# Optimization experiments

Hardware: AMD Instinct MI355X
Metric: run time of the kernel (lower is better)

## Reference

```python
import jax, jax.numpy as jnp
import numpy as np

BSZ, SEQ, DIM = 2, 2048, 4096
N_HEADS, N_KV_HEADS, HEAD_DIM = 32, 8, 128
N_REP = N_HEADS // N_KV_HEADS
MAX_BS, MAX_SEQ = 4, 2048
ROPE_THETA = 500000.0


def setup_inputs() -> dict:
    key = jax.random.key(0)
    ks = jax.random.split(key, 6)
    sc = 1.0 / np.sqrt(DIM)
    x = jax.random.normal(ks[0], (BSZ, SEQ, DIM), jnp.float32)
    wq = jax.random.normal(ks[1], (DIM, N_HEADS * HEAD_DIM), jnp.float32) * sc
    wk = jax.random.normal(ks[2], (DIM, N_KV_HEADS * HEAD_DIM), jnp.float32) * sc
    wv = jax.random.normal(ks[3], (DIM, N_KV_HEADS * HEAD_DIM), jnp.float32) * sc
    wo = jax.random.normal(ks[4], (N_HEADS * HEAD_DIM, DIM), jnp.float32) * sc
    cache_k = jnp.zeros((MAX_BS, MAX_SEQ, N_KV_HEADS, HEAD_DIM), jnp.float32)
    cache_v = jnp.zeros((MAX_BS, MAX_SEQ, N_KV_HEADS, HEAD_DIM), jnp.float32)
    # precomputed rotary frequencies (freqs_cis = cos + i*sin)
    inv = 1.0 / (ROPE_THETA ** (np.arange(0, HEAD_DIM, 2, dtype=np.float32) / HEAD_DIM))
    t = np.arange(SEQ, dtype=np.float32)
    freqs = np.outer(t, inv)  # [SEQ, HEAD_DIM//2]
    freqs_cos = jnp.asarray(np.cos(freqs), jnp.float32)
    freqs_sin = jnp.asarray(np.sin(freqs), jnp.float32)
    # causal additive mask, broadcast over (batch, heads)
    neg = jnp.full((SEQ, SEQ), -1e9, jnp.float32)
    mask = jnp.triu(neg, k=1)[None, None, :, :]
    return {"x": x, "wq": wq, "wk": wk, "wv": wv, "wo": wo,
            "cache_k": cache_k, "cache_v": cache_v,
            "freqs_cos": freqs_cos, "freqs_sin": freqs_sin,
            "mask": mask, "start_pos": 0}


def _apply_rope(t, cos, sin):
    # t: [b, s, h, d]; complex multiply on (even, odd) pairs
    b, s, h, d = t.shape
    tr = t.reshape(b, s, h, d // 2, 2)
    a, bb = tr[..., 0], tr[..., 1]
    cos = cos[None, :, None, :]
    sin = sin[None, :, None, :]
    out = jnp.stack([a * cos - bb * sin, a * sin + bb * cos], axis=-1)
    return out.reshape(b, s, h, d)


def reference(x, wq, wk, wv, wo, cache_k, cache_v, freqs_cos, freqs_sin, mask, start_pos):
    bsz, seqlen, _ = x.shape
    xq = (x @ wq).reshape(bsz, seqlen, N_HEADS, HEAD_DIM)
    xk = (x @ wk).reshape(bsz, seqlen, N_KV_HEADS, HEAD_DIM)
    xv = (x @ wv).reshape(bsz, seqlen, N_KV_HEADS, HEAD_DIM)
    xq = _apply_rope(xq, freqs_cos, freqs_sin)
    xk = _apply_rope(xk, freqs_cos, freqs_sin)
    # KV-cache append (start_pos is a static Python int)
    cache_k = jax.lax.dynamic_update_slice(cache_k, xk, (0, start_pos, 0, 0))
    cache_v = jax.lax.dynamic_update_slice(cache_v, xv, (0, start_pos, 0, 0))
    keys = cache_k[:bsz, : start_pos + seqlen]    # [b, kv_len, kvh, d]
    values = cache_v[:bsz, : start_pos + seqlen]
    # GQA repeat_kv: tile kv heads n_rep times -> [b, kv_len, H, d]
    keys = jnp.repeat(keys, N_REP, axis=2)
    values = jnp.repeat(values, N_REP, axis=2)
    q = xq.transpose(0, 2, 1, 3)        # [b, H, s, d]
    k = keys.transpose(0, 2, 1, 3)      # [b, H, kv, d]
    v = values.transpose(0, 2, 1, 3)
    scores = jnp.einsum('bhqd,bhkd->bhqk', q, k) / np.sqrt(HEAD_DIM)
    if mask is not None:
        scores = scores + mask
    probs = jax.nn.softmax(scores.astype(jnp.float32), axis=-1).astype(q.dtype)
    out = jnp.einsum('bhqk,bhkd->bhqd', probs, v)
    out = out.transpose(0, 2, 1, 3).reshape(bsz, seqlen, -1)
    return out @ wo
```

## Files before the change

kernel.cpp:

```cpp
#include <hip/hip_runtime.h>
#include <hip/hip_bf16.h>
#include <cstdint>

typedef __attribute__((ext_vector_type(8))) __bf16 bf16x8;
typedef __attribute__((ext_vector_type(4))) __bf16 bf16x4;
typedef __attribute__((ext_vector_type(2))) __bf16 bf16x2;
typedef __attribute__((ext_vector_type(4))) float  f32x4;

#define MFMA16(a,b,c) __builtin_amdgcn_mfma_f32_16x16x32_bf16((a),(b),(c),0,0,0)

__device__ __forceinline__ void gl16(const void* g, void* l) {
  __builtin_amdgcn_global_load_lds(
      (const __attribute__((address_space(1))) void*)g,
      (__attribute__((address_space(3))) void*)l, 16, 0, 0);
}

static constexpr int BSZ = 2, SEQ = 2048, DIM = 4096;
static constexpr int NH = 32, NKV = 8, HD = 128;
static constexpr int TOK = BSZ * SEQ;
static constexpr int NQKV = NH*HD + 2*NKV*HD;
static constexpr float QSCALE = 0.08838834764831845f;
static constexpr float FNEG = -3.0e38f;

__global__ __launch_bounds__(256) void f32_to_bf16_k(const float* __restrict__ in,
                                                     __bf16* __restrict__ out) {
  int i = (blockIdx.x * 256 + threadIdx.x) * 4;
  float4 v = *(const float4*)(in + i);
  bf16x4 o = { (__bf16)v.x, (__bf16)v.y, (__bf16)v.z, (__bf16)v.w };
  *(bf16x4*)(out + i) = o;
}

__global__ __launch_bounds__(256) void wtrans64_k(const float* __restrict__ S,
                                                  __bf16* __restrict__ D, int sC) {
  __shared__ __align__(16) __bf16 t[64 * 66];
  const int tid = threadIdx.x;
  const int cb = blockIdx.x, rb = blockIdx.y;
#pragma unroll
  for (int i = 0; i < 16; ++i) {
    int e = i * 256 + tid; int r = e >> 6, c = e & 63;
    t[c * 66 + r] = (__bf16)S[(size_t)(rb * 64 + r) * sC + cb * 64 + c];
  }
  __syncthreads();
#pragma unroll
  for (int i = 0; i < 16; ++i) {
    int e = i * 256 + tid; int c = e >> 6, r = e & 63;
    D[(size_t)(cb * 64 + c) * 4096 + rb * 64 + r] = t[c * 66 + r];
  }
}

__global__ __launch_bounds__(256) void gemm_bf16_bt_k(const __bf16* __restrict__ A,
                                                      const __bf16* __restrict__ Bt,
                                                      float* __restrict__ C,
                                                      int M, int N, int K) {
  __shared__ __align__(16) __bf16 lA[128 * 64];
  __shared__ __align__(16) __bf16 lB[128 * 64];
  const int tid = threadIdx.x, lane = tid & 63, wid = tid >> 6;
  const int bm = blockIdx.y, bn = blockIdx.x;
  const int wm = wid & 1, wn = wid >> 1;
  f32x4 acc[4][4] = {};

  const int srow = lane >> 3, scol = lane & 7;
  const __bf16* Ag = A + ((size_t)bm * 128 + wid * 8 + srow) * K + scol * 8;
  const __bf16* Bg = Bt + ((size_t)bn * 128 + wid * 8 + srow) * K + scol * 8;
  __bf16* lAw = lA + wid * 512;
  __bf16* lBw = lB + wid * 512;

  const int nk = K >> 6;
  for (int kt = 0; kt < nk; ++kt) {
    const __bf16* ag = Ag + (size_t)kt * 64;
    const __bf16* bg = Bg + (size_t)kt * 64;
#pragma unroll
    for (int i = 0; i < 4; ++i) {
      gl16(ag + (size_t)i * 32 * K, lAw + i * 2048);
      gl16(bg + (size_t)i * 32 * K, lBw + i * 2048);
    }
    __syncthreads();
#pragma unroll
    for (int kk = 0; kk < 2; ++kk) {
      bf16x8 af[4], bfv[4];
#pragma unroll
      for (int m = 0; m < 4; ++m)
        af[m] = *(const bf16x8*)&lA[(wm * 64 + m * 16 + (lane & 15)) * 64 + kk * 32 + (lane >> 4) * 8];
#pragma unroll
      for (int n = 0; n < 4; ++n)
        bfv[n] = *(const bf16x8*)&lB[(wn * 64 + n * 16 + (lane & 15)) * 64 + kk * 32 + (lane >> 4) * 8];
#pragma unroll
      for (int m = 0; m < 4; ++m)
#pragma unroll
        for (int n = 0; n < 4; ++n)
          acc[m][n] = MFMA16(af[m], bfv[n], acc[m][n]);
    }
    __syncthreads();
  }
  const int r0 = (lane >> 4) * 4, cN = lane & 15;
#pragma unroll
  for (int m = 0; m < 4; ++m) {
    size_t row = (size_t)bm * 128 + wm * 64 + m * 16 + r0;
#pragma unroll
    for (int n = 0; n < 4; ++n) {
      size_t col = (size_t)bn * 128 + wn * 64 + n * 16 + cN;
#pragma unroll
      for (int r = 0; r < 4; ++r)
        C[(row + r) * N + col] = acc[m][n][r];
    }
  }
}

__global__ __launch_bounds__(256) void rope_qk_k(const float* __restrict__ QKV,
                                                 const float* __restrict__ fc,
                                                 const float* __restrict__ fs,
                                                 __bf16* __restrict__ Qb,
                                                 __bf16* __restrict__ Kb) {
  int idx = blockIdx.x * 256 + threadIdx.x;
  int tok = idx / 2560;
  int rem = idx - tok * 2560;
  int head = rem >> 6, p = rem & 63;
  int b = tok >> 11, s = tok & 2047;
  float2 v = *(const float2*)(QKV + (size_t)tok * NQKV + head * 128 + 2 * p);
  float c = fc[s * 64 + p], sn = fs[s * 64 + p];
  float x = v.x * c - v.y * sn;
  float y = v.x * sn + v.y * c;
  if (head < 32) {
    x *= QSCALE; y *= QSCALE;
    bf16x2 o = { (__bf16)x, (__bf16)y };
    *(bf16x2*)(Qb + ((size_t)(b * 32 + head) * 2048 + s) * 128 + 2 * p) = o;
  } else {
    bf16x2 o = { (__bf16)x, (__bf16)y };
    *(bf16x2*)(Kb + ((size_t)(b * 8 + head - 32) * 2048 + s) * 128 + 2 * p) = o;
  }
}

__global__ __launch_bounds__(256) void vtrans_k(const float* __restrict__ QKV,
                                                __bf16* __restrict__ Vt) {
  __shared__ __align__(16) __bf16 t[128 * 66];
  const int sb = blockIdx.x, hk = blockIdx.y, b = blockIdx.z;
  const int tid = threadIdx.x;
#pragma unroll
  for (int i = 0; i < 32; ++i) {
    int e = i * 256 + tid; int s = e >> 7, d = e & 127;
    t[d * 66 + s] = (__bf16)QKV[(size_t)(b * 2048 + sb * 64 + s) * NQKV + 5120 + hk * 128 + d];
  }
  __syncthreads();
  int d = tid >> 1, s0 = (tid & 1) * 32;
  __bf16* dst = Vt + ((size_t)(b * 8 + hk) * 128 + d) * 2048 + sb * 64 + s0;
  const unsigned* srcu = (const unsigned*)&t[d * 66 + s0];
  unsigned* dstu = (unsigned*)dst;
#pragma unroll
  for (int i = 0; i < 16; ++i) dstu[i] = srcu[i];
}

__global__ __launch_bounds__(256) void attn64_k(const __bf16* __restrict__ Q,
                                                const __bf16* __restrict__ Kc,
                                                const __bf16* __restrict__ Vt,
                                                __bf16* __restrict__ Ab) {
  __shared__ __align__(16) __bf16 lK[64 * 128];
  __shared__ __align__(16) __bf16 lV[128 * 64];
  __shared__ __align__(16) __bf16 lP[4][16 * 64];
  const int qt = gridDim.x - 1 - blockIdx.x;
  const int h = blockIdx.y, b = blockIdx.z;
  const int hk = h >> 2;
  const int tid = threadIdx.x, lane = tid & 63, wid = tid >> 6;
  const int qb = qt * 64;
  const int lo = lane & 15, hi = lane >> 4;
  const int xk = (lo & 7) * 8;
  const __bf16* Qp = Q + ((size_t)(b * 32 + h) * 2048 + qb) * 128;
  const __bf16* Kp = Kc + (size_t)(b * 8 + hk) * 2048 * 128;
  const __bf16* Vp = Vt + (size_t)(b * 8 + hk) * 128 * 2048;

  bf16x8 qf[4];
#pragma unroll
  for (int kq = 0; kq < 4; ++kq)
    qf[kq] = *(const bf16x8*)(Qp + (size_t)(wid * 16 + lo) * 128 + kq * 32 + hi * 8);

  f32x4 accO[8] = {};
  float mr[4] = { FNEG, FNEG, FNEG, FNEG };
  float lr[4] = { 0.f, 0.f, 0.f, 0.f };

  const int srow16 = lane >> 4, scol16 = lane & 15;
  const int srow8 = lane >> 3, scol8 = lane & 7;

  for (int kb = 0; kb <= qt; ++kb) {
#pragma unroll
    for (int i = 0; i < 4; ++i) {
      const int krow = (i * 4 + wid) * 4 + srow16;
      gl16(Kp + (size_t)(kb * 64 + krow) * 128 + (scol16 ^ (krow & 7)) * 8,
           (__bf16*)lK + (i * 4 + wid) * 512);
      const int vrow = (i * 4 + wid) * 8 + srow8;
      gl16(Vp + (size_t)vrow * 2048 + kb * 64 + (scol8 ^ srow8) * 8,
           (__bf16*)lV + (i * 4 + wid) * 512);
    }
    __syncthreads();

    f32x4 sc[4] = {};
    __builtin_amdgcn_s_setprio(1);
#pragma unroll
    for (int nb = 0; nb < 4; ++nb)
#pragma unroll
      for (int kk = 0; kk < 4; ++kk) {
        bf16x8 kf = *(const bf16x8*)&lK[(nb * 16 + lo) * 128 + ((kk * 32 + hi * 8) ^ xk)];
        sc[nb] = MFMA16(qf[kk], kf, sc[nb]);
      }
    __builtin_amdgcn_s_setprio(0);

    const bool lastb = (kb == qt);
    const int qrow0 = qb + wid * 16 + hi * 4;
    const int kcol0 = kb * 64 + lo;
    float tm[4] = { FNEG, FNEG, FNEG, FNEG };
#pragma unroll
    for (int nb = 0; nb < 4; ++nb)
#pragma unroll
      for (int r = 0; r < 4; ++r) {
        float s = sc[nb][r];
        if (lastb && (kcol0 + nb * 16 > qrow0 + r)) s = FNEG;
        sc[nb][r] = s;
        tm[r] = fmaxf(tm[r], s);
      }
#pragma unroll
    for (int r = 0; r < 4; ++r) {
#pragma unroll
      for (int off = 1; off < 16; off <<= 1)
        tm[r] = fmaxf(tm[r], __shfl_xor(tm[r], off));
      float mn = fmaxf(mr[r], tm[r]);
      tm[r] = __expf(mr[r] - mn);
      mr[r] = mn;
    }
    float rs[4] = { 0.f, 0.f, 0.f, 0.f };
#pragma unroll
    for (int nb = 0; nb < 4; ++nb)
#pragma unroll
      for (int r = 0; r < 4; ++r) {
        float p = __expf(sc[nb][r] - mr[r]);
        rs[r] += p;
        const int q = hi * 4 + r;
        lP[wid][q * 64 + ((nb * 16 + lo) ^ ((q & 7) * 8))] = (__bf16)p;
      }
#pragma unroll
    for (int r = 0; r < 4; ++r) {
#pragma unroll
      for (int off = 1; off < 16; off <<= 1)
        rs[r] += __shfl_xor(rs[r], off);
      lr[r] = lr[r] * tm[r] + rs[r];
    }
#pragma unroll
    for (int nb2 = 0; nb2 < 8; ++nb2)
#pragma unroll
      for (int r = 0; r < 4; ++r)
        accO[nb2][r] *= tm[r];

    __syncthreads();

    __builtin_amdgcn_s_setprio(1);
#pragma unroll
    for (int kk = 0; kk < 2; ++kk) {
      bf16x8 pf = *(const bf16x8*)&lP[wid][lo * 64 + ((kk * 32 + hi * 8) ^ xk)];
#pragma unroll
      for (int nb2 = 0; nb2 < 8; ++nb2) {
        bf16x8 vf = *(const bf16x8*)&lV[(nb2 * 16 + lo) * 64 + ((kk * 32 + hi * 8) ^ xk)];
        accO[nb2] = MFMA16(pf, vf, accO[nb2]);
      }
    }
    __builtin_amdgcn_s_setprio(0);
    __syncthreads();
  }

  float inv[4];
#pragma unroll
  for (int r = 0; r < 4; ++r) inv[r] = 1.0f / lr[r];
#pragma unroll
  for (int nb2 = 0; nb2 < 8; ++nb2)
#pragma unroll
    for (int r = 0; r < 4; ++r)
      Ab[((size_t)b * 2048 + qb + wid * 16 + hi * 4 + r) * 4096 + h * 128 + nb2 * 16 + lo] =
          (__bf16)(accO[nb2][r] * inv[r]);
}

extern "C" void kernel_launch(void* const* d_in, const int* in_sizes, int n_in,
                              void* d_out, int out_size, void* d_ws, size_t ws_size,
                              hipStream_t stream) {
  const float* x  = (const float*)d_in[0];
  const float* wq = (const float*)d_in[1];
  const float* wk = (const float*)d_in[2];
  const float* wv = (const float*)d_in[3];
  const float* wo = (const float*)d_in[4];
  const float* fc = (const float*)d_in[7];
  const float* fs = (const float*)d_in[8];
  float* out = (float*)d_out;

  char* ws = (char*)d_ws;
  __bf16* Wqkvt = (__bf16*)(ws + 0);
  __bf16* Wot   = (__bf16*)(ws + 50331648);
  __bf16* Qb    = (__bf16*)(ws + 83886080);
  __bf16* Kb    = (__bf16*)(ws + 117440512);
  __bf16* Vtb   = (__bf16*)(ws + 125829120);
  __bf16* Xbf   = (__bf16*)(ws + 134217728);
  float*  QKVf  = (float*)(ws + 167772160);
  __bf16* Ab    = (__bf16*)(ws + 167772160);

  f32_to_bf16_k<<<TOK * DIM / 1024, 256, 0, stream>>>(x, Xbf);
  wtrans64_k<<<dim3(64, 64), 256, 0, stream>>>(wq, Wqkvt, 4096);
  wtrans64_k<<<dim3(16, 64), 256, 0, stream>>>(wk, Wqkvt + (size_t)4096 * 4096, 1024);
  wtrans64_k<<<dim3(16, 64), 256, 0, stream>>>(wv, Wqkvt + (size_t)5120 * 4096, 1024);
  wtrans64_k<<<dim3(64, 64), 256, 0, stream>>>(wo, Wot, 4096);

  gemm_bf16_bt_k<<<dim3(48, 32), 256, 0, stream>>>(Xbf, Wqkvt, QKVf, TOK, NQKV, DIM);

  rope_qk_k<<<TOK * 40 * 64 / 256, 256, 0, stream>>>(QKVf, fc, fs, Qb, Kb);
  vtrans_k<<<dim3(32, 8, 2), 256, 0, stream>>>(QKVf, Vtb);

  attn64_k<<<dim3(32, 32, 2), 256, 0, stream>>>(Qb, Kb, Vtb, Ab);

  gemm_bf16_bt_k<<<dim3(32, 32), 256, 0, stream>>>(Ab, Wot, out, TOK, DIM, DIM);
}
```

Measured before the change: 1.175 ms.

## Process 128-query tiles per block with double-buffered K/V prefetch

The attention kernel now handles two 64-row query sub-tiles per block, so each K/V tile loaded into LDS is reused twice. It double-buffers the K and V tiles, issuing the next tile's global-to-LDS load before computing on the current one, and drops one barrier per iteration. The cost is more registers (two accumulator sets) and more LDS. Causal work per block is also less balanced, and the grid has half as many blocks.

```diff
diff --git a/kernel.cpp b/kernel.cpp
--- a/kernel.cpp
+++ b/kernel.cpp
@@ -149,129 +149,150 @@
   for (int i = 0; i < 16; ++i) dstu[i] = srcu[i];
 }
 
-__global__ __launch_bounds__(256) void attn64_k(const __bf16* __restrict__ Q,
-                                                const __bf16* __restrict__ Kc,
-                                                const __bf16* __restrict__ Vt,
-                                                __bf16* __restrict__ Ab) {
-  __shared__ __align__(16) __bf16 lK[64 * 128];
-  __shared__ __align__(16) __bf16 lV[128 * 64];
+__global__ __launch_bounds__(256, 2) void attn128_k(const __bf16* __restrict__ Q,
+                                                    const __bf16* __restrict__ Kc,
+                                                    const __bf16* __restrict__ Vt,
+                                                    __bf16* __restrict__ Ab) {
+  __shared__ __align__(16) __bf16 lK[2][64 * 128];
+  __shared__ __align__(16) __bf16 lV[2][128 * 64];
   __shared__ __align__(16) __bf16 lP[4][16 * 64];
   const int qt = gridDim.x - 1 - blockIdx.x;
   const int h = blockIdx.y, b = blockIdx.z;
   const int hk = h >> 2;
   const int tid = threadIdx.x, lane = tid & 63, wid = tid >> 6;
-  const int qb = qt * 64;
+  const int qb = qt * 128;
   const int lo = lane & 15, hi = lane >> 4;
   const int xk = (lo & 7) * 8;
+  const int srow8 = lane >> 3, scol8 = lane & 7;
   const __bf16* Qp = Q + ((size_t)(b * 32 + h) * 2048 + qb) * 128;
   const __bf16* Kp = Kc + (size_t)(b * 8 + hk) * 2048 * 128;
   const __bf16* Vp = Vt + (size_t)(b * 8 + hk) * 128 * 2048;
 
-  bf16x8 qf[4];
-#pragma unroll
-  for (int kq = 0; kq < 4; ++kq)
-    qf[kq] = *(const bf16x8*)(Qp + (size_t)(wid * 16 + lo) * 128 + kq * 32 + hi * 8);
-
-  f32x4 accO[8] = {};
-  float mr[4] = { FNEG, FNEG, FNEG, FNEG };
-  float lr[4] = { 0.f, 0.f, 0.f, 0.f };
-
-  const int srow16 = lane >> 4, scol16 = lane & 15;
-  const int srow8 = lane >> 3, scol8 = lane & 7;
-
-  for (int kb = 0; kb <= qt; ++kb) {
+  bf16x8 qf[2][4];
+#pragma unroll
+  for (int rt = 0; rt < 2; ++rt)
+#pragma unroll
+    for (int kq = 0; kq < 4; ++kq)
+      qf[rt][kq] = *(const bf16x8*)(Qp + (size_t)(rt * 64 + wid * 16 + lo) * 128 + kq * 32 + hi * 8);
+
+  f32x4 accO[2][8] = {};
+  float mr[2][4] = { { FNEG, FNEG, FNEG, FNEG }, { FNEG, FNEG, FNEG, FNEG } };
+  float lr[2][4] = {};
+
+  const int nkb = 2 * qt + 2;
+
+  auto STAGE = [&](int t) {
+    const int kbase = t * 64;
+    __bf16* dK = lK[t & 1];
+    __bf16* dV = lV[t & 1];
 #pragma unroll
     for (int i = 0; i < 4; ++i) {
-      const int krow = (i * 4 + wid) * 4 + srow16;
-      gl16(Kp + (size_t)(kb * 64 + krow) * 128 + (scol16 ^ (krow & 7)) * 8,
-           (__bf16*)lK + (i * 4 + wid) * 512);
+      const int krow = (i * 4 + wid) * 4 + hi;
+      gl16(Kp + (size_t)(kbase + krow) * 128 + (lo ^ (krow & 7)) * 8,
+           dK + (i * 4 + wid) * 512);
       const int vrow = (i * 4 + wid) * 8 + srow8;
-      gl16(Vp + (size_t)vrow * 2048 + kb * 64 + (scol8 ^ srow8) * 8,
-           (__bf16*)lV + (i * 4 + wid) * 512);
-    }
-    __syncthreads();
-
-    f32x4 sc[4] = {};
-    __builtin_amdgcn_s_setprio(1);
-#pragma unroll
-    for (int nb = 0; nb < 4; ++nb)
-#pragma unroll
-      for (int kk = 0; kk < 4; ++kk) {
-        bf16x8 kf = *(const bf16x8*)&lK[(nb * 16 + lo) * 128 + ((kk * 32 + hi * 8) ^ xk)];
-        sc[nb] = MFMA16(qf[kk], kf, sc[nb]);
+      gl16(Vp + (size_t)vrow * 2048 + kbase + (scol8 ^ srow8) * 8,
+           dV + (i * 4 + wid) * 512);
+    }
+  };
+
+  STAGE(0);
+  asm volatile("s_waitcnt vmcnt(0)" ::: "memory");
+  __builtin_amdgcn_s_barrier();
+
+  for (int kb = 0; kb < nkb; ++kb) {
+    const int cur = kb & 1;
+    if (kb + 1 < nkb) STAGE(kb + 1);
+    const bool maskb = (kb >= nkb - 2);
+    const __bf16* bK = lK[cur];
+    const __bf16* bV = lV[cur];
+
+#pragma unroll
+    for (int rt = 0; rt < 2; ++rt) {
+      f32x4 sc[4] = {};
+      __builtin_amdgcn_s_setprio(1);
+#pragma unroll
+      for (int nb = 0; nb < 4; ++nb)
+#pragma unroll
+        for (int kk = 0; kk < 4; ++kk) {
+          bf16x8 kf = *(const bf16x8*)&bK[(nb * 16 + lo) * 128 + ((kk * 32 + hi * 8) ^ xk)];
+          sc[nb] = MFMA16(qf[rt][kk], kf, sc[nb]);
+        }
+      __builtin_amdgcn_s_setprio(0);
+
+      const int qrow0 = qb + rt * 64 + wid * 16 + hi * 4;
+      const int kcol0 = kb * 64 + lo;
+      float tm[4] = { FNEG, FNEG, FNEG, FNEG };
+#pragma unroll
+      for (int nb = 0; nb < 4; ++nb)
+#pragma unroll
+        for (int r = 0; r < 4; ++r) {
+          float s = sc[nb][r];
+          if (maskb && (kcol0 + nb * 16 > qrow0 + r)) s = FNEG;
+          sc[nb][r] = s;
+          tm[r] = fmaxf(tm[r], s);
+        }
+#pragma unroll
+      for (int r = 0; r < 4; ++r) {
+#pragma unroll
+        for (int off = 1; off < 16; off <<= 1)
+          tm[r] = fmaxf(tm[r], __shfl_xor(tm[r], off));
+        float mn = fmaxf(mr[rt][r], tm[r]);
+        tm[r] = __expf(mr[rt][r] - mn);
+        mr[rt][r] = mn;
       }
-    __builtin_amdgcn_s_setprio(0);
-
-    const bool lastb = (kb == qt);
-    const int qrow0 = qb + wid * 16 + hi * 4;
-    const int kcol0 = kb * 64 + lo;
-    float tm[4] = { FNEG, FNEG, FNEG, FNEG };
-#pragma unroll
-    for (int nb = 0; nb < 4; ++nb)
+      float rs[4] = {};
+#pragma unroll
+      for (int nb = 0; nb < 4; ++nb)
+#pragma unroll
+        for (int r = 0; r < 4; ++r) {
+          float p = __expf(sc[nb][r] - mr[rt][r]);
+          rs[r] += p;
+          const int q = hi * 4 + r;
+          lP[wid][q * 64 + ((nb * 16 + lo) ^ ((q & 7) * 8))] = (__bf16)p;
+        }
 #pragma unroll
       for (int r = 0; r < 4; ++r) {
-        float s = sc[nb][r];
-        if (lastb && (kcol0 + nb * 16 > qrow0 + r)) s = FNEG;
-        sc[nb][r] = s;
-        tm[r] = fmaxf(tm[r], s);
+#pragma unroll
+        for (int off = 1; off < 16; off <<= 1)
+          rs[r] += __shfl_xor(rs[r], off);
+        lr[rt][r] = lr[rt][r] * tm[r] + rs[r];
       }
 #pragma unroll
-    for (int r = 0; r < 4; ++r) {
-#pragma unroll
-      for (int off = 1; off < 16; off <<= 1)
-        tm[r] = fmaxf(tm[r], __shfl_xor(tm[r], off));
-      float mn = fmaxf(mr[r], tm[r]);
-      tm[r] = __expf(mr[r] - mn);
-      mr[r] = mn;
-    }
-    float rs[4] = { 0.f, 0.f, 0.f, 0.f };
-#pragma unroll
-    for (int nb = 0; nb < 4; ++nb)
-#pragma unroll
-      for (int r = 0; r < 4; ++r) {
-        float p = __expf(sc[nb][r] - mr[r]);
-        rs[r] += p;
-        const int q = hi * 4 + r;
-        lP[wid][q * 64 + ((nb * 16 + lo) ^ ((q & 7) * 8))] = (__bf16)p;
+      for (int nb2 = 0; nb2 < 8; ++nb2)
+#pragma unroll
+        for (int r = 0; r < 4; ++r)
+          accO[rt][nb2][r] *= tm[r];
+
+      __builtin_amdgcn_s_setprio(1);
+#pragma unroll
+      for (int kk = 0; kk < 2; ++kk) {
+        bf16x8 pf = *(const bf16x8*)&lP[wid][lo * 64 + ((kk * 32 + hi * 8) ^ xk)];
+#pragma unroll
+        for (int nb2 = 0; nb2 < 8; ++nb2) {
+          bf16x8 vf = *(const bf16x8*)&bV[(nb2 * 16 + lo) * 64 + ((kk * 32 + hi * 8) ^ xk)];
+          accO[rt][nb2] = MFMA16(pf, vf, accO[rt][nb2]);
+        }
       }
-#pragma unroll
-    for (int r = 0; r < 4; ++r) {
-#pragma unroll
-      for (int off = 1; off < 16; off <<= 1)
-        rs[r] += __shfl_xor(rs[r], off);
-      lr[r] = lr[r] * tm[r] + rs[r];
-    }
+      __builtin_amdgcn_s_setprio(0);
+    }
+
+    if (kb + 1 < nkb) asm volatile("s_waitcnt vmcnt(0)" ::: "memory");
+    __builtin_amdgcn_s_barrier();
+  }
+
+#pragma unroll
+  for (int rt = 0; rt < 2; ++rt) {
+    float inv[4];
+#pragma unroll
+    for (int r = 0; r < 4; ++r) inv[r] = 1.0f / lr[rt][r];
 #pragma unroll
     for (int nb2 = 0; nb2 < 8; ++nb2)
 #pragma unroll
       for (int r = 0; r < 4; ++r)
-        accO[nb2][r] *= tm[r];
-
-    __syncthreads();
-
-    __builtin_amdgcn_s_setprio(1);
-#pragma unroll
-    for (int kk = 0; kk < 2; ++kk) {
-      bf16x8 pf = *(const bf16x8*)&lP[wid][lo * 64 + ((kk * 32 + hi * 8) ^ xk)];
-#pragma unroll
-      for (int nb2 = 0; nb2 < 8; ++nb2) {
-        bf16x8 vf = *(const bf16x8*)&lV[(nb2 * 16 + lo) * 64 + ((kk * 32 + hi * 8) ^ xk)];
-        accO[nb2] = MFMA16(pf, vf, accO[nb2]);
-      }
-    }
-    __builtin_amdgcn_s_setprio(0);
-    __syncthreads();
-  }
-
-  float inv[4];
-#pragma unroll
-  for (int r = 0; r < 4; ++r) inv[r] = 1.0f / lr[r];
-#pragma unroll
-  for (int nb2 = 0; nb2 < 8; ++nb2)
-#pragma unroll
-    for (int r = 0; r < 4; ++r)
-      Ab[((size_t)b * 2048 + qb + wid * 16 + hi * 4 + r) * 4096 + h * 128 + nb2 * 16 + lo] =
-          (__bf16)(accO[nb2][r] * inv[r]);
+        Ab[((size_t)b * 2048 + qb + rt * 64 + wid * 16 + hi * 4 + r) * 4096 + h * 128 + nb2 * 16 + lo] =
+            (__bf16)(accO[rt][nb2][r] * inv[r]);
+  }
 }
 
 extern "C" void kernel_launch(void* const* d_in, const int* in_sizes, int n_in,
@@ -307,7 +328,7 @@
   rope_qk_k<<<TOK * 40 * 64 / 256, 256, 0, stream>>>(QKVf, fc, fs, Qb, Kb);
   vtrans_k<<<dim3(32, 8, 2), 256, 0, stream>>>(QKVf, Vtb);
 
-  attn64_k<<<dim3(32, 32, 2), 256, 0, stream>>>(Qb, Kb, Vtb, Ab);
+  attn128_k<<<dim3(16, 32, 2), 256, 0, stream>>>(Qb, Kb, Vtb, Ab);
 
   gemm_bf16_bt_k<<<dim3(32, 32), 256, 0, stream>>>(Ab, Wot, out, TOK, DIM, DIM);
 }
```

Result: faster. 1.124 ms (-4.4%).
